# Optimization experiments

Measured on AMD Instinct MI355X. Metric: run time of the kernel, lower is better.

Reference implementation:

```python
import jax, jax.numpy as jnp
import numpy as np

B, S, D = 4, 1024, 2048
NH, HD = 16, 128  # nhead, head_dim
SCALE = HD ** -0.5


def setup_inputs() -> dict:
    key = jax.random.key(0)
    ks = jax.random.split(key, 7)
    query = jax.random.normal(ks[0], (B, S, D), dtype=jnp.float32)
    key_t = jax.random.normal(ks[1], (B, S, D), dtype=jnp.float32)
    value = jax.random.normal(ks[2], (B, S, D), dtype=jnp.float32)
    # qkv_proj: Linear(D, 3D) with bias; out_proj: Linear(D, D) with bias
    Wqkv = jax.random.normal(ks[3], (3 * D, D), dtype=jnp.float32) * (D ** -0.5)
    bqkv = jnp.zeros((3 * D,), dtype=jnp.float32)
    Wout = jax.random.normal(ks[4], (D, D), dtype=jnp.float32) * (D ** -0.5)
    bout = jnp.zeros((D,), dtype=jnp.float32)
    return {"query": query, "key": key_t, "value": value,
            "Wqkv": Wqkv, "bqkv": bqkv, "Wout": Wout, "bout": bout}


def reference(query, key, value, Wqkv, bqkv, Wout, bout):
    # NOTE: module ignores `key`/`value` args; qkv comes from query alone.
    b, s, d = query.shape
    qkv = query @ Wqkv.T + bqkv                       # (B,S,3D)
    q, k, v = jnp.split(qkv, 3, axis=-1)
    q = q.reshape(b, s, NH, HD).transpose(0, 2, 1, 3) * SCALE  # (B,H,S,hd)
    k = k.reshape(b, s, NH, HD).transpose(0, 2, 1, 3)          # (B,H,S,hd)
    # faithful replication of the module's odd v permutation:
    v = v.reshape(b, s, HD, NH).transpose(0, 2, 1, 3)          # (B,hd,S,H)
    v = v.reshape(b, s, NH * HD).reshape(b, s, NH, HD).transpose(0, 2, 1, 3)  # (B,H,S,hd)
    scores = jnp.einsum('bhqd,bhkd->bhqk', q, k)               # (B,H,S,S)
    causal = jnp.triu(jnp.ones((s, s), dtype=bool), k=1)
    scores = jnp.where(causal, -jnp.inf, scores)
    attn = jax.nn.softmax(scores.astype(jnp.float32), axis=-1).astype(query.dtype)
    out = jnp.einsum('bhqk,bhkd->bhqd', attn, v)               # (B,H,S,hd)
    out = out.transpose(0, 2, 1, 3).reshape(b, s, d)
    return out @ Wout.T + bout
```

## Files before the change

kernel.cpp:

```cpp
#include <hip/hip_runtime.h>
#include <hip/hip_bf16.h>
#include <stdint.h>

typedef __bf16 bf16x8 __attribute__((ext_vector_type(8)));
typedef float  floatx4 __attribute__((ext_vector_type(4)));

#define NEG_BIG (-1e30f)

#define GLD16(g, l) __builtin_amdgcn_global_load_lds(                         \
    (__attribute__((address_space(1))) void*)(g),                             \
    (__attribute__((address_space(3))) void*)(l), 16, 0, 0)

__device__ __forceinline__ void cvt16(const float* __restrict__ s,
                                      __hip_bfloat16* __restrict__ d) {
    float4 f[4];
#pragma unroll
    for (int i = 0; i < 4; i++) f[i] = ((const float4*)s)[i];
    union { __hip_bfloat16 h[16]; uint4 u[2]; } o;
#pragma unroll
    for (int i = 0; i < 4; i++) {
        o.h[4 * i + 0] = __float2bfloat16(f[i].x);
        o.h[4 * i + 1] = __float2bfloat16(f[i].y);
        o.h[4 * i + 2] = __float2bfloat16(f[i].z);
        o.h[4 * i + 3] = __float2bfloat16(f[i].w);
    }
    ((uint4*)d)[0] = o.u[0];
    ((uint4*)d)[1] = o.u[1];
}

__global__ __launch_bounds__(256)
void cvt3_f32_bf16(const float* __restrict__ a, size_t na8,
                   const float* __restrict__ b, size_t nb8,
                   const float* __restrict__ c, size_t nc8,
                   __hip_bfloat16* __restrict__ da,
                   __hip_bfloat16* __restrict__ db,
                   __hip_bfloat16* __restrict__ dc)
{
    const size_t total  = na8 + nb8 + nc8;
    const size_t stride = (size_t)gridDim.x * blockDim.x;
    for (size_t idx = (size_t)blockIdx.x * blockDim.x + threadIdx.x;
         idx < total; idx += stride) {
        const float* s; __hip_bfloat16* d; size_t o;
        if (idx < na8)            { s = a; d = da; o = idx; }
        else if (idx < na8 + nb8) { s = b; d = db; o = idx - na8; }
        else                      { s = c; d = dc; o = idx - na8 - nb8; }
        const float4 f0 = ((const float4*)s)[o * 2 + 0];
        const float4 f1 = ((const float4*)s)[o * 2 + 1];
        union { __hip_bfloat16 h[8]; uint4 u; } z;
        z.h[0] = __float2bfloat16(f0.x); z.h[1] = __float2bfloat16(f0.y);
        z.h[2] = __float2bfloat16(f0.z); z.h[3] = __float2bfloat16(f0.w);
        z.h[4] = __float2bfloat16(f1.x); z.h[5] = __float2bfloat16(f1.y);
        z.h[6] = __float2bfloat16(f1.z); z.h[7] = __float2bfloat16(f1.w);
        ((uint4*)d)[o] = z.u;
    }
}

template <bool A_F32, bool B_F32, bool OUT_F32>
__global__ __launch_bounds__(256, 2)
void gemm_nt_bias(const void* __restrict__ Av, const void* __restrict__ Bv,
                  const float* __restrict__ bias, void* __restrict__ Cv,
                  int M, int N, int K, int lda, int ldb)
{
    __shared__ __align__(16) __hip_bfloat16 Asm[128 * 32];
    __shared__ __align__(16) __hip_bfloat16 Bsm[128 * 32];
    const int m0   = blockIdx.y * 128;
    const int n0   = blockIdx.x * 128;
    const int t    = threadIdx.x;
    const int wave = t >> 6, lane = t & 63;
    const int quad = lane >> 4, l16 = lane & 15;
    const int wr   = wave >> 1, wc = wave & 1;

    floatx4 zero = {0.f, 0.f, 0.f, 0.f};
    floatx4 acc[4][4];
    for (int i = 0; i < 4; i++)
        for (int j = 0; j < 4; j++) acc[i][j] = zero;

    for (int k0 = 0; k0 < K; k0 += 32) {
        if (A_F32) {
            const float* A = (const float*)Av;
            const int row = t >> 1, half = t & 1;
            cvt16(A + (size_t)(m0 + row) * lda + k0 + half * 16,
                  Asm + row * 32 + half * 16);
        } else {
            const __hip_bfloat16* A = (const __hip_bfloat16*)Av;
            for (int j = 0; j < 2; ++j) {
                const int chunk = (wave * 2 + j) * 64 + lane;
                const int row   = chunk >> 2;
                const int kc    = chunk & 3;
                GLD16(A + (size_t)(m0 + row) * lda + k0 + kc * 8,
                      Asm + (wave * 2 + j) * 512);
            }
        }
        if (B_F32) {
            const float* B = (const float*)Bv;
            const int row = t >> 1, half = t & 1;
            cvt16(B + (size_t)(n0 + row) * ldb + k0 + half * 16,
                  Bsm + row * 32 + half * 16);
        } else {
            const __hip_bfloat16* B = (const __hip_bfloat16*)Bv;
            for (int j = 0; j < 2; ++j) {
                const int chunk = (wave * 2 + j) * 64 + lane;
                const int row   = chunk >> 2;
                const int kc    = chunk & 3;
                GLD16(B + (size_t)(n0 + row) * ldb + k0 + kc * 8,
                      Bsm + (wave * 2 + j) * 512);
            }
        }
        __syncthreads();

        bf16x8 af[4], bf[4];
        for (int i = 0; i < 4; i++) {
            af[i] = *(const bf16x8*)(Asm + (wr * 64 + i * 16 + l16) * 32 + quad * 8);
            bf[i] = *(const bf16x8*)(Bsm + (wc * 64 + i * 16 + l16) * 32 + quad * 8);
        }
        for (int mi = 0; mi < 4; mi++)
            for (int ni = 0; ni < 4; ni++)
                acc[mi][ni] = __builtin_amdgcn_mfma_f32_16x16x32_bf16(
                    af[mi], bf[ni], acc[mi][ni], 0, 0, 0);
        __syncthreads();
    }

    for (int mi = 0; mi < 4; mi++) {
        const int row = m0 + wr * 64 + mi * 16 + quad * 4;
        for (int ni = 0; ni < 4; ni++) {
            const int col = n0 + wc * 64 + ni * 16 + l16;
            const float bv = bias[col];
            for (int r = 0; r < 4; r++) {
                const float v = acc[mi][ni][r] + bv;
                if (OUT_F32)
                    ((float*)Cv)[(size_t)(row + r) * N + col] = v;
                else
                    ((__hip_bfloat16*)Cv)[(size_t)(row + r) * N + col] =
                        __float2bfloat16(v);
            }
        }
    }
}

__global__ __launch_bounds__(256)
void permute_v(const __hip_bfloat16* __restrict__ QKV,
               __hip_bfloat16* __restrict__ Vpt)
{
    __shared__ __align__(16) __hip_bfloat16 S[64 * 64];
    const int blk = blockIdx.x;
    const int sb = blk & 31, h = (blk >> 5) & 15, b = blk >> 9;
    const int t = threadIdx.x;

    for (int j = 0; j < 2; j++) {
        const int chunk = j * 256 + t;
        const int lrow  = chunk >> 3;
        const int lcol  = (chunk & 7) * 8;
        const int r8 = lrow >> 3, jj = lrow & 7;
        const int srow = r8 * 128 + h * 8 + jj;
        const int scol = sb * 64 + lcol;
        *(uint4*)(S + chunk * 8) =
            *(const uint4*)(QKV + ((size_t)(b * 1024) + srow) * 6144 + 4096 + scol);
    }
    __syncthreads();

    const size_t obase = (((size_t)(b * 16 + h)) * 32 + sb) * 4096;
    for (int i = 0; i < 16; i++) {
        const int lin = t + 256 * i;
        const int hd = lin >> 5, ss = lin & 31;
        Vpt[obase + lin] =
            S[((ss & 7) * 8 + (hd >> 4)) * 64 + (ss >> 3) * 16 + (hd & 15)];
    }
}

__global__ __launch_bounds__(256, 2)
void flash_attn(const __hip_bfloat16* __restrict__ QKV,
                const __hip_bfloat16* __restrict__ Vpt,
                __hip_bfloat16* __restrict__ O)
{
    __shared__ __align__(16) __hip_bfloat16 Kt[2][64 * 128];
    __shared__ __align__(16) __hip_bfloat16 Vt[2][2 * 128 * 32];
    __shared__ __align__(16) __hip_bfloat16 Pl[64 * 64];

    const int bid  = blockIdx.x;
    const int pair = bid >> 6;
    const int g    = bid & 63;
    const int b    = g >> 4, h = g & 15;
    const int t    = threadIdx.x;
    const int wave = t >> 6, lane = t & 63;
    const int quad = lane >> 4, l16 = lane & 15;
    const float scale = 0.08838834764831845f;

    const int    rowb  = b * 1024;
    const size_t vbase = (((size_t)(b * 16 + h)) * 32) * 4096;
    const floatx4 zero = {0.f, 0.f, 0.f, 0.f};

    auto stageK = [&](int tk, int bufi) {
        const int kv0 = tk * 64;
        __hip_bfloat16* dst = &Kt[bufi][0];
#pragma unroll
        for (int j = 0; j < 4; j++) {
            const int c0 = (wave * 4 + j) * 64 + lane;
            const int r  = c0 >> 4;
            const int gg = (c0 & 15) ^ (r & 7);
            GLD16(QKV + ((size_t)(rowb + kv0 + r)) * 6144 + 2048 + h * 128 + gg * 8,
                  dst + (wave * 4 + j) * 512);
        }
    };
    auto stageV = [&](int tk, int bufi) {
        const __hip_bfloat16* src = Vpt + vbase + (size_t)(tk * 2) * 4096;
        __hip_bfloat16* dst = &Vt[bufi][0];
#pragma unroll
        for (int j = 0; j < 4; j++) {
            const int c0   = (wave * 4 + j) * 64 + lane;
            const int half = c0 >> 9, w = c0 & 511;
            const int r    = w >> 2;
            const int gg   = (w & 3) ^ (r & 3);
            GLD16(src + half * 4096 + r * 32 + gg * 8,
                  dst + (wave * 4 + j) * 512);
        }
    };

    for (int ph = 0; ph < 2; ++ph) {
        const int qb = ph ? (15 - pair) * 64 : pair * 64;
        const int nt = ph ? 16 - pair       : pair + 1;

        bf16x8 qf[4];
        {
            const size_t rb = ((size_t)(rowb + qb + wave * 16 + l16)) * 6144 + h * 128;
#pragma unroll
            for (int kc = 0; kc < 4; kc++)
                qf[kc] = *(const bf16x8*)(QKV + rb + kc * 32 + quad * 8);
        }

        float m_i[4], l_i[4];
        floatx4 oacc[8];
#pragma unroll
        for (int r = 0; r < 4; r++) { m_i[r] = NEG_BIG; l_i[r] = 0.f; }
#pragma unroll
        for (int ni = 0; ni < 8; ni++) oacc[ni] = zero;

        stageK(0, 0); stageV(0, 0);

        for (int tk = 0; tk < nt; ++tk) {
            const int cur = tk & 1;
            if (tk + 1 < nt) {
                stageK(tk + 1, cur ^ 1); stageV(tk + 1, cur ^ 1);
                asm volatile("s_waitcnt vmcnt(8)" ::: "memory");
            } else {
                asm volatile("s_waitcnt vmcnt(0)" ::: "memory");
            }
            __builtin_amdgcn_s_barrier();
            asm volatile("" ::: "memory");

            const __hip_bfloat16* Kb = &Kt[cur][0];
            const __hip_bfloat16* Vb = &Vt[cur][0];
            const int kv0 = tk * 64;

            floatx4 sc[4];
#pragma unroll
            for (int cb = 0; cb < 4; cb++) {
                floatx4 s = zero;
                const int r  = cb * 16 + l16;
                const int sw = r & 7;
#pragma unroll
                for (int kc = 0; kc < 4; kc++) {
                    bf16x8 kf = *(const bf16x8*)(
                        Kb + r * 128 + (((kc * 4 + quad) ^ sw) << 3));
                    s = __builtin_amdgcn_mfma_f32_16x16x32_bf16(qf[kc], kf, s, 0, 0, 0);
                }
                sc[cb] = s;
            }

            const int qrow = qb + wave * 16 + quad * 4;
            if (tk == nt - 1) {
#pragma unroll
                for (int rr = 0; rr < 4; rr++)
#pragma unroll
                    for (int cb = 0; cb < 4; cb++) {
                        const int col = kv0 + cb * 16 + l16;
                        const float v = sc[cb][rr] * scale;
                        sc[cb][rr] = (col > qrow + rr) ? NEG_BIG : v;
                    }
            } else {
#pragma unroll
                for (int rr = 0; rr < 4; rr++)
#pragma unroll
                    for (int cb = 0; cb < 4; cb++) sc[cb][rr] *= scale;
            }
            float mx[4];
#pragma unroll
            for (int rr = 0; rr < 4; rr++)
                mx[rr] = fmaxf(fmaxf(sc[0][rr], sc[1][rr]),
                               fmaxf(sc[2][rr], sc[3][rr]));
#pragma unroll
            for (int off = 1; off < 16; off <<= 1)
#pragma unroll
                for (int rr = 0; rr < 4; rr++)
                    mx[rr] = fmaxf(mx[rr], __shfl_xor(mx[rr], off));

            float alpha[4], rsum[4];
#pragma unroll
            for (int rr = 0; rr < 4; rr++) {
                const float mnew = fmaxf(m_i[rr], mx[rr]);
                alpha[rr] = __expf(m_i[rr] - mnew);
                m_i[rr] = mnew;
                float acc = 0.f;
#pragma unroll
                for (int cb = 0; cb < 4; cb++) {
                    const float pv = __expf(sc[cb][rr] - mnew);
                    sc[cb][rr] = pv;
                    acc += pv;
                }
                rsum[rr] = acc;
            }
#pragma unroll
            for (int off = 1; off < 16; off <<= 1)
#pragma unroll
                for (int rr = 0; rr < 4; rr++)
                    rsum[rr] += __shfl_xor(rsum[rr], off);
#pragma unroll
            for (int rr = 0; rr < 4; rr++)
                l_i[rr] = l_i[rr] * alpha[rr] + rsum[rr];
#pragma unroll
            for (int ni = 0; ni < 8; ni++)
#pragma unroll
                for (int rr = 0; rr < 4; rr++) oacc[ni][rr] *= alpha[rr];

#pragma unroll
            for (int cb = 0; cb < 4; cb++)
#pragma unroll
                for (int rr = 0; rr < 4; rr++) {
                    const int row = wave * 16 + quad * 4 + rr;
                    const int col = cb * 16 + l16;
                    Pl[row * 64 + ((((col >> 3) ^ (row & 7)) << 3) | (col & 7))] =
                        __float2bfloat16(sc[cb][rr]);
                }
            asm volatile("s_waitcnt lgkmcnt(0)" ::: "memory");

            const int prow = wave * 16 + l16;
            bf16x8 pf[2];
#pragma unroll
            for (int kc = 0; kc < 2; kc++)
                pf[kc] = *(const bf16x8*)(
                    Pl + prow * 64 + (((kc * 4 + quad) ^ (prow & 7)) << 3));
#pragma unroll
            for (int ni = 0; ni < 8; ni++) {
                const int vr = ni * 16 + l16;
#pragma unroll
                for (int kc = 0; kc < 2; kc++) {
                    bf16x8 vf = *(const bf16x8*)(
                        Vb + kc * 4096 + vr * 32 + (((quad ^ (vr & 3))) << 3));
                    oacc[ni] = __builtin_amdgcn_mfma_f32_16x16x32_bf16(
                        pf[kc], vf, oacc[ni], 0, 0, 0);
                }
            }

            asm volatile("" ::: "memory");
            __builtin_amdgcn_s_barrier();
            asm volatile("" ::: "memory");
        }

        float inv[4];
#pragma unroll
        for (int rr = 0; rr < 4; rr++) inv[rr] = 1.0f / l_i[rr];
#pragma unroll
        for (int ni = 0; ni < 8; ni++)
#pragma unroll
            for (int rr = 0; rr < 4; rr++) {
                const int row = qb + wave * 16 + quad * 4 + rr;
                O[((size_t)rowb + row) * 6144 + 4096 + h * 128 + ni * 16 + l16] =
                    __float2bfloat16(oacc[ni][rr] * inv[rr]);
            }
    }
}

extern "C" void kernel_launch(void* const* d_in, const int* in_sizes, int n_in,
                              void* d_out, int out_size, void* d_ws, size_t ws_size,
                              hipStream_t stream) {
    const float* query = (const float*)d_in[0];
    const float* Wqkv = (const float*)d_in[3];
    const float* bqkv = (const float*)d_in[4];
    const float* Wout = (const float*)d_in[5];
    const float* bout = (const float*)d_in[6];
    float* out = (float*)d_out;

    const size_t MB = 1048576;
    char* ws = (char*)d_ws;
    __hip_bfloat16* QKV = (__hip_bfloat16*)ws;
    __hip_bfloat16* Vpt = (__hip_bfloat16*)(ws + 48 * MB);
    __hip_bfloat16* Att = QKV + 4096;

    dim3 blk(256);

    if (ws_size >= 113 * MB) {
        __hip_bfloat16* Qbf     = (__hip_bfloat16*)(ws + 64 * MB);
        __hip_bfloat16* Wqkv_bf = (__hip_bfloat16*)(ws + 80 * MB);
        __hip_bfloat16* Wout_bf = (__hip_bfloat16*)(ws + 104 * MB);

        cvt3_f32_bf16<<<dim3(2048), blk, 0, stream>>>(
            query, (size_t)4096 * 2048 / 8,
            Wqkv,  (size_t)6144 * 2048 / 8,
            Wout,  (size_t)2048 * 2048 / 8,
            Qbf, Wqkv_bf, Wout_bf);
        gemm_nt_bias<false, false, false><<<dim3(48, 32), blk, 0, stream>>>(
            Qbf, Wqkv_bf, bqkv, QKV, 4096, 6144, 2048, 2048, 2048);
        permute_v<<<dim3(2048), blk, 0, stream>>>(QKV, Vpt);
        flash_attn<<<dim3(512), blk, 0, stream>>>(QKV, Vpt, QKV);
        gemm_nt_bias<false, false, true><<<dim3(16, 32), blk, 0, stream>>>(
            Att, Wout_bf, bout, out, 4096, 2048, 2048, 6144, 2048);
    } else {
        gemm_nt_bias<true, true, false><<<dim3(48, 32), blk, 0, stream>>>(
            query, Wqkv, bqkv, QKV, 4096, 6144, 2048, 2048, 2048);
        permute_v<<<dim3(2048), blk, 0, stream>>>(QKV, Vpt);
        flash_attn<<<dim3(512), blk, 0, stream>>>(QKV, Vpt, QKV);
        gemm_nt_bias<false, true, true><<<dim3(16, 32), blk, 0, stream>>>(
            Att, Wout, bout, out, 4096, 2048, 2048, 6144, 2048);
    }
}
```

Measured before the change: 390.4 us.

## Add 256x256-tile pipelined bf16 GEMM for the QKV projection

Adds a new GEMM kernel with 256x256 output tiles, 512 threads, BK=64 and double-buffered LDS. Global-to-LDS loads are interleaved with the MFMA phases and run up to two k-steps ahead. The kernel also uses an XOR-swizzled LDS layout, grid swizzling for L2 locality, and s_setprio around MFMA bursts. It replaces the 128x128 GEMM for the QKV projection to raise data reuse per tile and hide load latency. In exchange it uses 128KB of LDS per block and many accumulator registers, and the grid has only 384 workgroups, which limits occupancy and may cause wave-quantization imbalance.

```diff
diff --git a/kernel.cpp b/kernel.cpp
--- a/kernel.cpp
+++ b/kernel.cpp
@@ -55,6 +55,144 @@
     }
 }
 
+template <bool OUT_F32>
+__global__ __launch_bounds__(512, 2)
+void gemm256_nt_bias(const __hip_bfloat16* __restrict__ A,
+                     const __hip_bfloat16* __restrict__ B,
+                     const float* __restrict__ bias, void* __restrict__ Cv,
+                     int M, int N, int K, int lda, int ldb, int nbx)
+{
+    __shared__ __align__(16) __hip_bfloat16 Asm[2][256 * 64];
+    __shared__ __align__(16) __hip_bfloat16 Bsm[2][256 * 64];
+
+    const int nwg = gridDim.x, cpx = nwg >> 3;
+    const int flat = blockIdx.x;
+    const int swz  = (flat & 7) * cpx + (flat >> 3);
+    const int bx = swz % nbx, by = swz / nbx;
+    const int m0 = by * 256, n0 = bx * 256;
+
+    const int t    = threadIdx.x;
+    const int wave = t >> 6, lane = t & 63;
+    const int quad = lane >> 4, l16 = lane & 15;
+    const int wr   = wave >> 2, wc = wave & 3;
+    const int NT   = K >> 6;
+
+    const int s_   = wave >> 2;
+    const int w3   = wave & 3;
+    const int l8   = lane >> 3;
+    const int g_   = (lane & 7) ^ l8;
+    const __hip_bfloat16* aSrc = A + (size_t)(m0 + s_ * 128 + w3 * 8 + l8) * lda + g_ * 8;
+    const __hip_bfloat16* bSrc = B + (size_t)(n0 + wave * 8 + l8) * ldb + g_ * 8;
+
+    auto stageA = [&](int tk, int b, int buf) {
+        GLD16(aSrc + (size_t)(b * 32) * lda + tk * 64,
+              &Asm[buf][0] + (s_ * 128 + b * 32 + w3 * 8) * 64);
+    };
+    auto stageBhalf = [&](int tk, int h, int buf) {
+#pragma unroll
+        for (int j = 0; j < 2; j++)
+            GLD16(bSrc + (size_t)(h * 128 + j * 64) * ldb + tk * 64,
+                  &Bsm[buf][0] + (h * 128 + j * 64 + wave * 8) * 64);
+    };
+
+    const int g0 = (quad ^ (l16 & 7)) << 3;
+
+    floatx4 acc[8][4];
+    const floatx4 zero = {0.f, 0.f, 0.f, 0.f};
+#pragma unroll
+    for (int mi = 0; mi < 8; mi++)
+#pragma unroll
+        for (int ni = 0; ni < 4; ni++) acc[mi][ni] = zero;
+
+    stageA(0, 0, 0); stageA(0, 1, 0); stageA(0, 2, 0); stageA(0, 3, 0);
+    stageBhalf(0, 0, 0); stageBhalf(0, 1, 0);
+    if (NT > 1) {
+        stageA(1, 0, 1); stageA(1, 1, 1); stageA(1, 2, 1);
+        asm volatile("s_waitcnt vmcnt(3)" ::: "memory");
+    } else {
+        asm volatile("s_waitcnt vmcnt(0)" ::: "memory");
+    }
+    __syncthreads();
+
+    bf16x8 bfr[4][2];
+    int cb = 0;
+    for (int tk = 0; tk < NT; ++tk, cb ^= 1) {
+        const __hip_bfloat16* Ab = &Asm[cb][0];
+        const __hip_bfloat16* Bb = &Bsm[cb][0];
+        const int nb = cb ^ 1;
+
+#pragma unroll
+        for (int p = 0; p < 4; p++) {
+            bf16x8 af[2][2];
+#pragma unroll
+            for (int i = 0; i < 2; i++)
+#pragma unroll
+                for (int ks = 0; ks < 2; ks++)
+                    af[i][ks] = *(const bf16x8*)(
+                        Ab + (wr * 128 + (2 * p + i) * 16 + l16) * 64 +
+                        (g0 ^ (ks ? 32 : 0)));
+            if (p == 0) {
+#pragma unroll
+                for (int ni = 0; ni < 4; ni++)
+#pragma unroll
+                    for (int ks = 0; ks < 2; ks++)
+                        bfr[ni][ks] = *(const bf16x8*)(
+                            Bb + (wc * 64 + ni * 16 + l16) * 64 +
+                            (g0 ^ (ks ? 32 : 0)));
+            }
+            if (p == 0) {
+                if (tk + 1 < NT) { stageA(tk + 1, 3, nb); stageBhalf(tk + 1, 0, nb); }
+            } else if (p == 1) {
+                if (tk + 1 < NT) stageBhalf(tk + 1, 1, nb);
+                if (tk + 2 < NT) stageA(tk + 2, 0, cb);
+            } else if (p == 2) {
+                if (tk + 2 < NT) stageA(tk + 2, 1, cb);
+            } else {
+                if (tk + 2 < NT) stageA(tk + 2, 2, cb);
+            }
+
+            __builtin_amdgcn_s_barrier();
+            asm volatile("s_waitcnt lgkmcnt(0)" ::: "memory");
+            __builtin_amdgcn_s_setprio(1);
+#pragma unroll
+            for (int ks = 0; ks < 2; ks++)
+#pragma unroll
+                for (int i = 0; i < 2; i++)
+#pragma unroll
+                    for (int ni = 0; ni < 4; ni++)
+                        acc[2 * p + i][ni] = __builtin_amdgcn_mfma_f32_16x16x32_bf16(
+                            af[i][ks], bfr[ni][ks], acc[2 * p + i][ni], 0, 0, 0);
+            __builtin_amdgcn_s_setprio(0);
+            if (p == 3) {
+                if (tk + 2 < NT)
+                    asm volatile("s_waitcnt vmcnt(3)" ::: "memory");
+                else if (tk + 1 < NT)
+                    asm volatile("s_waitcnt vmcnt(0)" ::: "memory");
+            }
+            __builtin_amdgcn_s_barrier();
+        }
+    }
+
+#pragma unroll
+    for (int mi = 0; mi < 8; mi++) {
+        const int row = m0 + wr * 128 + mi * 16 + quad * 4;
+#pragma unroll
+        for (int ni = 0; ni < 4; ni++) {
+            const int col = n0 + wc * 64 + ni * 16 + l16;
+            const float bv = bias[col];
+#pragma unroll
+            for (int r = 0; r < 4; r++) {
+                const float v = acc[mi][ni][r] + bv;
+                if (OUT_F32)
+                    ((float*)Cv)[(size_t)(row + r) * N + col] = v;
+                else
+                    ((__hip_bfloat16*)Cv)[(size_t)(row + r) * N + col] =
+                        __float2bfloat16(v);
+            }
+        }
+    }
+}
+
 template <bool A_F32, bool B_F32, bool OUT_F32>
 __global__ __launch_bounds__(256, 2)
 void gemm_nt_bias(const void* __restrict__ Av, const void* __restrict__ Bv,
@@ -253,9 +391,9 @@
 
             floatx4 sc[4];
 #pragma unroll
-            for (int cb = 0; cb < 4; cb++) {
+            for (int cbk = 0; cbk < 4; cbk++) {
                 floatx4 s = zero;
-                const int r  = cb * 16 + l16;
+                const int r  = cbk * 16 + l16;
                 const int sw = r & 7;
 #pragma unroll
                 for (int kc = 0; kc < 4; kc++) {
@@ -263,7 +401,7 @@
                         Kb + r * 128 + (((kc * 4 + quad) ^ sw) << 3));
                     s = __builtin_amdgcn_mfma_f32_16x16x32_bf16(qf[kc], kf, s, 0, 0, 0);
                 }
-                sc[cb] = s;
+                sc[cbk] = s;
             }
 
             const int qrow = qb + wave * 16 + quad * 4;
@@ -271,16 +409,16 @@
 #pragma unroll
                 for (int rr = 0; rr < 4; rr++)
 #pragma unroll
-                    for (int cb = 0; cb < 4; cb++) {
-                        const int col = kv0 + cb * 16 + l16;
-                        const float v = sc[cb][rr] * scale;
-                        sc[cb][rr] = (col > qrow + rr) ? NEG_BIG : v;
+                    for (int cbk = 0; cbk < 4; cbk++) {
+                        const int col = kv0 + cbk * 16 + l16;
+                        const float v = sc[cbk][rr] * scale;
+                        sc[cbk][rr] = (col > qrow + rr) ? NEG_BIG : v;
                     }
             } else {
 #pragma unroll
                 for (int rr = 0; rr < 4; rr++)
 #pragma unroll
-                    for (int cb = 0; cb < 4; cb++) sc[cb][rr] *= scale;
+                    for (int cbk = 0; cbk < 4; cbk++) sc[cbk][rr] *= scale;
             }
             float mx[4];
 #pragma unroll
@@ -301,9 +439,9 @@
                 m_i[rr] = mnew;
                 float acc = 0.f;
 #pragma unroll
-                for (int cb = 0; cb < 4; cb++) {
-                    const float pv = __expf(sc[cb][rr] - mnew);
-                    sc[cb][rr] = pv;
+                for (int cbk = 0; cbk < 4; cbk++) {
+                    const float pv = __expf(sc[cbk][rr] - mnew);
+                    sc[cbk][rr] = pv;
                     acc += pv;
                 }
                 rsum[rr] = acc;
@@ -322,13 +460,13 @@
                 for (int rr = 0; rr < 4; rr++) oacc[ni][rr] *= alpha[rr];
 
 #pragma unroll
-            for (int cb = 0; cb < 4; cb++)
+            for (int cbk = 0; cbk < 4; cbk++)
 #pragma unroll
                 for (int rr = 0; rr < 4; rr++) {
                     const int row = wave * 16 + quad * 4 + rr;
-                    const int col = cb * 16 + l16;
+                    const int col = cbk * 16 + l16;
                     Pl[row * 64 + ((((col >> 3) ^ (row & 7)) << 3) | (col & 7))] =
-                        __float2bfloat16(sc[cb][rr]);
+                        __float2bfloat16(sc[cbk][rr]);
                 }
             asm volatile("s_waitcnt lgkmcnt(0)" ::: "memory");
 
@@ -397,8 +535,8 @@
             Wqkv,  (size_t)6144 * 2048 / 8,
             Wout,  (size_t)2048 * 2048 / 8,
             Qbf, Wqkv_bf, Wout_bf);
-        gemm_nt_bias<false, false, false><<<dim3(48, 32), blk, 0, stream>>>(
-            Qbf, Wqkv_bf, bqkv, QKV, 4096, 6144, 2048, 2048, 2048);
+        gemm256_nt_bias<false><<<dim3(384), dim3(512), 0, stream>>>(
+            Qbf, Wqkv_bf, bqkv, QKV, 4096, 6144, 2048, 2048, 2048, 24);
         permute_v<<<dim3(2048), blk, 0, stream>>>(QKV, Vpt);
         flash_attn<<<dim3(512), blk, 0, stream>>>(QKV, Vpt, QKV);
         gemm_nt_bias<false, false, true><<<dim3(16, 32), blk, 0, stream>>>(
```

Result: no change. 388.6 us (-0.5%).
